# Kernel optimization log

Measured on AMD Instinct MI355X. Metric: run time of the kernel, lower is better.

Reference implementation:

```python
import jax, jax.numpy as jnp
from jax import lax
import numpy as np

NUM_BLOCK, NUM_LAYER = 4, 10
DILATIONS = [2 ** (i % NUM_LAYER) for i in range(NUM_BLOCK * NUM_LAYER)]


def setup_inputs() -> dict:
    key = jax.random.key(0)
    ks = jax.random.split(key, 6)
    s = 0.05
    return {
        "x": jax.random.normal(ks[0], (8, 256, 16000), dtype=jnp.float32),
        "W_start": jax.random.normal(ks[1], (32, 256), dtype=jnp.float32) * s,
        "W_dil": jax.random.normal(ks[2], (40, 128, 32, 2), dtype=jnp.float32) * s,
        "W_res": jax.random.normal(ks[3], (40, 32, 128), dtype=jnp.float32) * s,
        "W_e1": jax.random.normal(ks[4], (256, 32), dtype=jnp.float32) * s,
        "W_e2": jax.random.normal(ks[5], (256, 256), dtype=jnp.float32) * s,
    }


def _causal_dilated_conv(x, w, dilation):
    # x: [B, Cin, T], w: [Cout, Cin, K=2]. Left-pad (K-1)*dilation -> causal,
    # equivalent to torch symmetric-pad-then-trim-right.
    pad = (w.shape[-1] - 1) * dilation
    return lax.conv_general_dilated(
        x, w, window_strides=(1,), padding=[(pad, 0)],
        rhs_dilation=(dilation,), dimension_numbers=("NCH", "OIH", "NCH"))


def reference(x, W_start, W_dil, W_res, W_e1, W_e2):
    # start 1x1 conv (no bias)
    residual = jnp.einsum("oc,bct->bot", W_start, x)  # [B,32,T]
    skips = jnp.zeros_like(residual)
    for i, d in enumerate(DILATIONS):
        h = _causal_dilated_conv(residual, W_dil[i], d)       # [B,128,T]
        g = jnp.tanh(h) * jax.nn.sigmoid(h)                   # gated activation
        skip = jnp.einsum("oc,bct->bot", W_res[i], g)         # 1x1 -> [B,32,T]
        residual = residual + skip
        skips = skips + skip
    h = jax.nn.relu(skips)
    h = jax.nn.relu(jnp.einsum("oc,bct->bot", W_e1, h))       # [B,256,T]
    logits = jnp.einsum("oc,bct->bot", W_e2, h)               # [B,256,T]
    return logits
```

## Files before the change

kernel.cpp:

```cpp
#include <hip/hip_runtime.h>
#include <math.h>

#define T_LEN 16000
#define NTILE 250
#define TT 64
#define NBLK 2000
#define LGRID 500

static const int N_RES = 8 * 32 * T_LEN;

typedef _Float16 half_t;
typedef __attribute__((ext_vector_type(8))) _Float16 halfx8;
typedef __attribute__((ext_vector_type(4))) _Float16 halfx4;
typedef __attribute__((ext_vector_type(16))) float f32x16;
typedef unsigned int uint32;
typedef unsigned short ushort16;

#define MFMA(a, b, c) __builtin_amdgcn_mfma_f32_32x32x16_f16((a), (b), (c), 0, 0, 0)

static __device__ inline uint32 packpair(float a, float b) {
  half_t ha = (half_t)a, hb = (half_t)b;
  return (uint32)__builtin_bit_cast(ushort16, ha) |
         ((uint32)__builtin_bit_cast(ushort16, hb) << 16);
}

__global__ __launch_bounds__(256) void repack_k(
    const float* __restrict__ Wd, const float* __restrict__ Wr,
    const float* __restrict__ Ws, const float* __restrict__ We1,
    const float* __restrict__ We2,
    half_t* __restrict__ WaG, half_t* __restrict__ WrG, float* __restrict__ WsT,
    half_t* __restrict__ We1S, half_t* __restrict__ We2S) {
  int i = blockIdx.x * 256 + threadIdx.x;
  if (i < 40 * 128 * 128) {
    int l = i >> 14, r = i & 16383, o = r >> 7, k = r & 127;
    int kk = k & 63, c = kk >> 1, s = kk & 1;
    float w = Wd[(((l * 128 + o) * 32 + c) << 1) + s];
    half_t w0 = (half_t)w;
    WaG[i] = (k < 64) ? w0 : (half_t)((w - (float)w0) * 2048.f);
  }
  if (i < 40 * 32 * 256) {
    int l = i >> 13, r = i & 8191, o2 = r >> 8, k = r & 255;
    int kk = k & 127;
    int ks = kk >> 4, lh = (kk >> 3) & 1, j = kk & 7;
    int mh = ks >> 2, til = (ks >> 1) & 1, ab = ks & 1;
    int m = mh * 64 + til * 32 + ab * 16 + (j & 3) + ((j >> 2) << 3) + lh * 4;
    float w = Wr[(l * 32 + o2) * 128 + m];
    half_t w0 = (half_t)w;
    WrG[i] = (k < 128) ? w0 : (half_t)((w - (float)w0) * 2048.f);
  }
  if (i < 8192) {
    int c = i >> 5, o = i & 31;
    WsT[i] = Ws[o * 256 + c];
  }
  if (i < 16384) {
    int o = i >> 6, k = i & 63;
    float w = We1[o * 32 + (k & 31)];
    half_t w0 = (half_t)w;
    We1S[i] = (k < 32) ? w0 : (half_t)((w - (float)w0) * 2048.f);
  }
  if (i < 131072) {
    int o = i >> 9, k = i & 511;
    float w = We2[o * 256 + (k & 255)];
    half_t w0 = (half_t)w;
    We2S[i] = (k < 256) ? w0 : (half_t)((w - (float)w0) * 2048.f);
  }
}

__global__ __launch_bounds__(256) void start_k(const float* __restrict__ x,
                                               const float* __restrict__ WsT,
                                               float* __restrict__ res) {
  __shared__ float xs[32][68];
  int b = blockIdx.x / NTILE;
  int t0 = (blockIdx.x % NTILE) * TT;
  int tid = threadIdx.x;
  int o = tid & 31, tg = (tid >> 5) * 8;
  int lr = tid >> 3, lt = (tid & 7) * 8;
  float acc[8];
#pragma unroll
  for (int j = 0; j < 8; ++j) acc[j] = 0.f;
  for (int cc = 0; cc < 8; ++cc) {
    __syncthreads();
    const float* xp = x + ((size_t)b * 256 + cc * 32 + lr) * T_LEN + t0 + lt;
    *(float4*)&xs[lr][lt]     = *(const float4*)xp;
    *(float4*)&xs[lr][lt + 4] = *(const float4*)(xp + 4);
    __syncthreads();
#pragma unroll 4
    for (int c = 0; c < 32; ++c) {
      float w = WsT[(cc * 32 + c) * 32 + o];
      const float* xr = &xs[c][tg];
#pragma unroll
      for (int j = 0; j < 8; ++j) acc[j] += w * xr[j];
    }
  }
  float* rp = res + ((size_t)b * 32 + o) * T_LEN + t0 + tg;
  *(float4*)rp       = make_float4(acc[0], acc[1], acc[2], acc[3]);
  *(float4*)(rp + 4) = make_float4(acc[4], acc[5], acc[6], acc[7]);
}

__global__ __launch_bounds__(256, 3) void layer_k(const float* __restrict__ resIn,
                                                  float* __restrict__ resOut,
                                                  const half_t* __restrict__ WaL,
                                                  const half_t* __restrict__ WrL, int d) {
  __shared__ __align__(16) char sm[26112];
  const int ZT_OFF = 0, SKB_OFF = 0, CUR_OFF = 17408;
  int tid = threadIdx.x;
  int wave = tid >> 6, lane = tid & 63;
  int l31 = lane & 31, lhi = lane >> 5;
  int mh = wave & 1, nh = wave >> 1;

  for (int ti = 0; ti < 4; ++ti) {
    int tile = blockIdx.x + ti * LGRID;
    int b = tile / NTILE;
    int t0 = (tile - b * NTILE) * TT;

    {
      int c = tid >> 3, tw = (tid & 7) * 8;
      const float* rip = resIn + ((size_t)b * 32 + c) * T_LEN;
      float cv[8], pv[8];
      *(float4*)cv       = *(const float4*)(rip + t0 + tw);
      *(float4*)(cv + 4) = *(const float4*)(rip + t0 + tw + 4);
      int tp = t0 + tw - d;
      if (tp >= 0 && (d & 3) == 0) {
        *(float4*)pv       = *(const float4*)(rip + tp);
        *(float4*)(pv + 4) = *(const float4*)(rip + tp + 4);
      } else {
#pragma unroll
        for (int j = 0; j < 8; ++j) {
          int q = tp + j;
          pv[j] = (q >= 0) ? rip[q] : 0.f;
        }
      }
      float* cw = (float*)(sm + CUR_OFF) + c * 68 + tw;
      *(float4*)cw       = *(const float4*)cv;
      *(float4*)(cw + 4) = *(const float4*)(cv + 4);
#pragma unroll
      for (int j = 0; j < 8; ++j) {
        int t = tw + j;
        int sw = ((t >> 3) & 3) << 5;
        char* zrow = sm + ZT_OFF + t * 272;
        half_t p0 = (half_t)pv[j];
        half_t c0 = (half_t)cv[j];
        float pl = (pv[j] - (float)p0) * 2048.f;
        float cl = (cv[j] - (float)c0) * 2048.f;
        *(uint32*)(zrow + ((c * 4) ^ sw))       = packpair(pv[j], cv[j]);
        *(uint32*)(zrow + ((c * 4 + 128) ^ sw)) = packpair(pl, cl);
      }
    }
    __syncthreads();

    halfx8 a1h0[4], a1l0[4], a1h1[4], a1l1[4];
    {
      const half_t* wa = WaL + (mh * 64 + l31) * 128 + lhi * 8;
#pragma unroll
      for (int j = 0; j < 4; ++j) {
        a1h0[j] = *(const halfx8*)(wa + j * 16);
        a1l0[j] = *(const halfx8*)(wa + 64 + j * 16);
        a1h1[j] = *(const halfx8*)(wa + 32 * 128 + j * 16);
        a1l1[j] = *(const halfx8*)(wa + 32 * 128 + 64 + j * 16);
      }
    }

    f32x16 hi0{}, hi1{}, lo0{}, lo1{};
    {
      int colt = nh * 32 + l31;
      int sw = ((colt >> 3) & 3) << 5;
      const char* zr = sm + ZT_OFF + colt * 272;
#pragma unroll
      for (int ks = 0; ks < 12; ++ks) {
        int brow = (ks < 4) ? ks * 16 : ((ks < 8) ? (ks & 3) * 16 + 64 : (ks & 3) * 16);
        halfx8 bf = *(const halfx8*)(zr + ((brow * 2 + lhi * 16) ^ sw));
        if (ks < 4) {
          hi0 = MFMA(a1h0[ks], bf, hi0);
          hi1 = MFMA(a1h1[ks], bf, hi1);
        } else if (ks < 8) {
          lo0 = MFMA(a1h0[ks & 3], bf, lo0);
          lo1 = MFMA(a1h1[ks & 3], bf, lo1);
        } else {
          lo0 = MFMA(a1l0[ks & 3], bf, lo0);
          lo1 = MFMA(a1l1[ks & 3], bf, lo1);
        }
      }
    }

    halfx8 wrHi[4], wrLo[4];
    {
      const half_t* wr = WrL + l31 * 256 + mh * 64 + lhi * 8;
#pragma unroll
      for (int q = 0; q < 4; ++q) {
        wrHi[q] = *(const halfx8*)(wr + q * 16);
        wrLo[q] = *(const halfx8*)(wr + 128 + q * 16);
      }
    }

    halfx8 gh0a, gh0b, gl0a, gl0b, gh1a, gh1b, gl1a, gl1b;
    {
#pragma unroll
      for (int r = 0; r < 16; ++r) {
        float ha = hi0[r] + lo0[r] * (1.f / 2048.f);
        float hb = hi1[r] + lo1[r] * (1.f / 2048.f);
        ha = fmaxf(ha, -30.f);
        hb = fmaxf(hb, -30.f);
        float ea = __expf(-ha), eb = __expf(-hb);
        float ga = (1.f - ea) * __builtin_amdgcn_rcpf(1.f + ea * ea);
        float gb = (1.f - eb) * __builtin_amdgcn_rcpf(1.f + eb * eb);
        half_t ga0 = (half_t)ga;
        half_t gb0 = (half_t)gb;
        half_t ga1 = (half_t)((ga - (float)ga0) * 2048.f);
        half_t gb1 = (half_t)((gb - (float)gb0) * 2048.f);
        if (r < 8) {
          gh0a[r] = ga0; gl0a[r] = ga1; gh1a[r] = gb0; gl1a[r] = gb1;
        } else {
          gh0b[r - 8] = ga0; gl0b[r - 8] = ga1; gh1b[r - 8] = gb0; gl1b[r - 8] = gb1;
        }
      }
    }

    f32x16 shi{}, slo{};
    {
      shi = MFMA(wrHi[0], gh0a, shi);
      shi = MFMA(wrHi[1], gh0b, shi);
      shi = MFMA(wrHi[2], gh1a, shi);
      shi = MFMA(wrHi[3], gh1b, shi);
      slo = MFMA(wrHi[0], gl0a, slo);
      slo = MFMA(wrHi[1], gl0b, slo);
      slo = MFMA(wrHi[2], gl1a, slo);
      slo = MFMA(wrHi[3], gl1b, slo);
      slo = MFMA(wrLo[0], gh0a, slo);
      slo = MFMA(wrLo[1], gh0b, slo);
      slo = MFMA(wrLo[2], gh1a, slo);
      slo = MFMA(wrLo[3], gh1b, slo);
    }
    __syncthreads();

    {
      float* skb = (float*)(sm + SKB_OFF) + mh * 32 * 68;
#pragma unroll
      for (int r = 0; r < 16; ++r) {
        int row = (r & 3) + 8 * (r >> 2) + 4 * lhi;
        skb[row * 68 + nh * 32 + l31] = shi[r] + slo[r] * (1.f / 2048.f);
      }
    }
    __syncthreads();

    {
      int c = tid >> 3, tw = (tid & 7) * 8;
      const float* s0 = (const float*)(sm + SKB_OFF) + c * 68 + tw;
      const float* s1 = s0 + 32 * 68;
      const float* cu = (const float*)(sm + CUR_OFF) + c * 68 + tw;
      size_t base = ((size_t)b * 32 + c) * T_LEN + t0 + tw;
#pragma unroll
      for (int v = 0; v < 8; v += 4) {
        float4 sa = *(const float4*)(s0 + v);
        float4 sb = *(const float4*)(s1 + v);
        float4 cv = *(const float4*)(cu + v);
        float4 o;
        o.x = cv.x + sa.x + sb.x;
        o.y = cv.y + sa.y + sb.y;
        o.z = cv.z + sa.z + sb.z;
        o.w = cv.w + sa.w + sb.w;
        *(float4*)(resOut + base + v) = o;
      }
    }
    __syncthreads();
  }
}

__global__ __launch_bounds__(512) void end_k(const float* __restrict__ resF,
                                             const float* __restrict__ res0,
                                             const half_t* __restrict__ We1S,
                                             const half_t* __restrict__ We2S,
                                             float* __restrict__ out) {
  __shared__ __align__(16) char sm[75776];
  const int H2T_OFF = 0, H1F_OFF = 0, H1T_OFF = 66560;
  int tid = threadIdx.x;
  int b = blockIdx.x / NTILE;
  int t0 = (blockIdx.x % NTILE) * TT;

  {
    int c = tid >> 4, tt4 = (tid & 15) * 4;
    size_t base = ((size_t)b * 32 + c) * T_LEN + t0 + tt4;
    float4 f = *(const float4*)(resF + base);
    float4 z = *(const float4*)(res0 + base);
    float* h1 = (float*)(sm + H1F_OFF) + c * 68 + tt4;
    h1[0] = fmaxf(f.x - z.x, 0.f);
    h1[1] = fmaxf(f.y - z.y, 0.f);
    h1[2] = fmaxf(f.z - z.z, 0.f);
    h1[3] = fmaxf(f.w - z.w, 0.f);
  }
  __syncthreads();
  {
    int t = tid & 63, cg = tid >> 6;
    const float* h1 = (const float*)(sm + H1F_OFF);
    halfx4 hi, lo;
#pragma unroll
    for (int j = 0; j < 4; ++j) {
      float v = h1[(cg * 4 + j) * 68 + t];
      half_t h = (half_t)v;
      hi[j] = h;
      lo[j] = (half_t)((v - (float)h) * 2048.f);
    }
    half_t* h1t = (half_t*)(sm + H1T_OFF) + t * 72;
    *(halfx4*)(h1t + cg * 4)      = hi;
    *(halfx4*)(h1t + 32 + cg * 4) = lo;
  }
  __syncthreads();

  int wave = tid >> 6, lane = tid & 63;
  int l31 = lane & 31, lhi = lane >> 5;

  f32x16 aHi0{}, aHi1{}, aLo0{}, aLo1{};
  {
    const char* h1t = sm + H1T_OFF;
    const half_t* wp = We1S + (wave * 32 + l31) * 64;
#pragma unroll
    for (int ks = 0; ks < 2; ++ks) {
      halfx8 hiA = *(const halfx8*)(wp + ks * 16 + lhi * 8);
      halfx8 loA = *(const halfx8*)(wp + 32 + ks * 16 + lhi * 8);
      const char* br0 = h1t + l31 * 144;
      const char* br1 = h1t + (32 + l31) * 144;
      halfx8 hiB0 = *(const halfx8*)(br0 + (ks * 16 + lhi * 8) * 2);
      halfx8 loB0 = *(const halfx8*)(br0 + (32 + ks * 16 + lhi * 8) * 2);
      halfx8 hiB1 = *(const halfx8*)(br1 + (ks * 16 + lhi * 8) * 2);
      halfx8 loB1 = *(const halfx8*)(br1 + (32 + ks * 16 + lhi * 8) * 2);
      aHi0 = MFMA(hiA, hiB0, aHi0);
      aLo0 = MFMA(hiA, loB0, aLo0);
      aLo0 = MFMA(loA, hiB0, aLo0);
      aHi1 = MFMA(hiA, hiB1, aHi1);
      aLo1 = MFMA(hiA, loB1, aLo1);
      aLo1 = MFMA(loA, hiB1, aLo1);
    }
  }
  {
#pragma unroll
    for (int n = 0; n < 2; ++n) {
      const f32x16& aH = n ? aHi1 : aHi0;
      const f32x16& aL = n ? aLo1 : aLo0;
      int t = n * 32 + l31;
      half_t* row = (half_t*)(sm + H2T_OFF) + t * 520;
#pragma unroll
      for (int g = 0; g < 4; ++g) {
        halfx4 hi, lo;
#pragma unroll
        for (int j = 0; j < 4; ++j) {
          int r = g * 4 + j;
          float v = aH[r] + aL[r] * (1.f / 2048.f);
          v = fmaxf(v, 0.f);
          half_t h = (half_t)v;
          hi[j] = h;
          lo[j] = (half_t)((v - (float)h) * 2048.f);
        }
        int col = wave * 32 + g * 8 + lhi * 4;
        *(halfx4*)(row + col)       = hi;
        *(halfx4*)(row + 256 + col) = lo;
      }
    }
  }
  __syncthreads();

  f32x16 bHi0{}, bHi1{}, bLo0{}, bLo1{};
  {
    const half_t* wp = We2S + (size_t)(wave * 32 + l31) * 512;
    const char* h2t = sm + H2T_OFF;
#pragma unroll 2
    for (int ks = 0; ks < 16; ++ks) {
      halfx8 hiA = *(const halfx8*)(wp + ks * 16 + lhi * 8);
      halfx8 loA = *(const halfx8*)(wp + 256 + ks * 16 + lhi * 8);
      const char* br0 = h2t + l31 * 1040;
      const char* br1 = h2t + (32 + l31) * 1040;
      halfx8 hiB0 = *(const halfx8*)(br0 + (ks * 16 + lhi * 8) * 2);
      halfx8 loB0 = *(const halfx8*)(br0 + (256 + ks * 16 + lhi * 8) * 2);
      halfx8 hiB1 = *(const halfx8*)(br1 + (ks * 16 + lhi * 8) * 2);
      halfx8 loB1 = *(const halfx8*)(br1 + (256 + ks * 16 + lhi * 8) * 2);
      bHi0 = MFMA(hiA, hiB0, bHi0);
      bLo0 = MFMA(hiA, loB0, bLo0);
      bLo0 = MFMA(loA, hiB0, bLo0);
      bHi1 = MFMA(hiA, hiB1, bHi1);
      bLo1 = MFMA(hiA, loB1, bLo1);
      bLo1 = MFMA(loA, hiB1, bLo1);
    }
  }
  {
#pragma unroll
    for (int n = 0; n < 2; ++n) {
      const f32x16& bH = n ? bHi1 : bHi0;
      const f32x16& bL = n ? bLo1 : bLo0;
      int t = t0 + n * 32 + l31;
#pragma unroll
      for (int r = 0; r < 16; ++r) {
        int o = wave * 32 + (r & 3) + 8 * (r >> 2) + 4 * lhi;
        out[((size_t)b * 256 + o) * T_LEN + t] = bH[r] + bL[r] * (1.f / 2048.f);
      }
    }
  }
}

extern "C" void kernel_launch(void* const* d_in, const int* in_sizes, int n_in,
                              void* d_out, int out_size, void* d_ws, size_t ws_size,
                              hipStream_t stream) {
  const float* x   = (const float*)d_in[0];
  const float* Wst = (const float*)d_in[1];
  const float* Wd  = (const float*)d_in[2];
  const float* Wr  = (const float*)d_in[3];
  const float* We1 = (const float*)d_in[4];
  const float* We2 = (const float*)d_in[5];
  float* out = (float*)d_out;
  float* ws = (float*)d_ws;

  float* resA = ws;
  float* resB = resA + N_RES;
  float* resC = resB + N_RES;
  half_t* WaG  = (half_t*)(resC + N_RES);
  half_t* WrG  = WaG + 40 * 16384;
  float*  WsT  = (float*)(WrG + 40 * 8192);
  half_t* We1S = (half_t*)(WsT + 8192);
  half_t* We2S = We1S + 16384;

  repack_k<<<2560, 256, 0, stream>>>(Wd, Wr, Wst, We1, We2, WaG, WrG, WsT, We1S, We2S);
  start_k<<<NBLK, 256, 0, stream>>>(x, WsT, resA);

  const float* rin = resA;
  for (int l = 0; l < 40; ++l) {
    float* rout = (l & 1) ? resC : resB;
    layer_k<<<LGRID, 256, 0, stream>>>(rin, rout, WaG + l * 16384, WrG + l * 8192,
                                       1 << (l % 10));
    rin = rout;
  }
  end_k<<<NBLK, 512, 0, stream>>>(rin, resA, We1S, We2S, out);
}
```

Before: 1.183 ms.

## Prefetch next tile's residual into registers and hoist weight loads out of tile loop

The per-layer kernel now loads the layer weights into registers once, before the tile loop, instead of reloading them for every tile. It double-buffers the current and previous-time residual values in registers, so the global load for the next tile is issued while the MFMA work on the current tile runs. The residual is kept in registers rather than a shared-memory copy, which shrinks LDS use. Launch bounds drop from 3 to 2 blocks per SM to leave room for the extra registers, which may reduce occupancy.

```diff
diff --git a/kernel.cpp b/kernel.cpp
--- a/kernel.cpp
+++ b/kernel.cpp
@@ -97,172 +97,177 @@
   *(float4*)(rp + 4) = make_float4(acc[4], acc[5], acc[6], acc[7]);
 }
 
-__global__ __launch_bounds__(256, 3) void layer_k(const float* __restrict__ resIn,
+#define LOAD_TILE(TI, CV, PV)                                              \
+  {                                                                        \
+    int tl_ = blockIdx.x + (TI) * LGRID;                                   \
+    int bb_ = tl_ / NTILE;                                                 \
+    int tb_ = (tl_ - bb_ * NTILE) * TT;                                    \
+    const float* rip_ = resIn + ((size_t)bb_ * 32 + cth) * T_LEN;          \
+    *(float4*)(CV)       = *(const float4*)(rip_ + tb_ + twh);             \
+    *(float4*)((CV) + 4) = *(const float4*)(rip_ + tb_ + twh + 4);         \
+    int tp_ = tb_ + twh - d;                                               \
+    if (tp_ >= 0 && (d & 3) == 0) {                                        \
+      *(float4*)(PV)       = *(const float4*)(rip_ + tp_);                 \
+      *(float4*)((PV) + 4) = *(const float4*)(rip_ + tp_ + 4);             \
+    } else {                                                               \
+      _Pragma("unroll")                                                    \
+      for (int j_ = 0; j_ < 8; ++j_) {                                     \
+        int q_ = tp_ + j_;                                                 \
+        (PV)[j_] = (q_ >= 0) ? rip_[q_] : 0.f;                             \
+      }                                                                    \
+    }                                                                      \
+  }
+
+#define TILE_BODY(TI, CV, PV, NCV, NPV, PREF)                                  \
+  {                                                                            \
+    int tile = blockIdx.x + (TI) * LGRID;                                      \
+    int b = tile / NTILE;                                                      \
+    int t0 = (tile - b * NTILE) * TT;                                          \
+                                             \
+    _Pragma("unroll")                                                          \
+    for (int j = 0; j < 8; ++j) {                                              \
+      int t = twh + j;                                                         \
+      int sw = ((t >> 3) & 3) << 5;                                            \
+      char* zrow = sm + t * 272;                                               \
+      half_t p0 = (half_t)(PV)[j];                                             \
+      half_t c0 = (half_t)(CV)[j];                                             \
+      float pl = ((PV)[j] - (float)p0) * 2048.f;                               \
+      float cl = ((CV)[j] - (float)c0) * 2048.f;                               \
+      *(uint32*)(zrow + ((cth * 4) ^ sw))       = packpair((PV)[j], (CV)[j]);  \
+      *(uint32*)(zrow + ((cth * 4 + 128) ^ sw)) = packpair(pl, cl);            \
+    }                                                                          \
+    __syncthreads();                                                           \
+       \
+    if (PREF) { LOAD_TILE((TI) + 1, NCV, NPV); }                               \
+                                      \
+    f32x16 hi0{}, hi1{}, lo0{}, lo1{};                                         \
+    {                                                                          \
+      int colt = nh * 32 + l31;                                                \
+      int sw = ((colt >> 3) & 3) << 5;                                         \
+      const char* zr = sm + colt * 272;                                        \
+      _Pragma("unroll")                                                        \
+      for (int ks = 0; ks < 12; ++ks) {                                        \
+        int brow = (ks < 4) ? ks * 16                                          \
+                            : ((ks < 8) ? (ks & 3) * 16 + 64 : (ks & 3) * 16); \
+        halfx8 bf = *(const halfx8*)(zr + ((brow * 2 + lhi * 16) ^ sw));       \
+        if (ks < 4) {                                                          \
+          hi0 = MFMA(a1h0[ks], bf, hi0);                                       \
+          hi1 = MFMA(a1h1[ks], bf, hi1);                                       \
+        } else if (ks < 8) {                                                   \
+          lo0 = MFMA(a1h0[ks & 3], bf, lo0);                                   \
+          lo1 = MFMA(a1h1[ks & 3], bf, lo1);                                   \
+        } else {                                                               \
+          lo0 = MFMA(a1l0[ks & 3], bf, lo0);                                   \
+          lo1 = MFMA(a1l1[ks & 3], bf, lo1);                                   \
+        }                                                                      \
+      }                                                                        \
+    }                                                                          \
+                          \
+    halfx8 gh0a, gh0b, gl0a, gl0b, gh1a, gh1b, gl1a, gl1b;                     \
+    _Pragma("unroll")                                                          \
+    for (int r = 0; r < 16; ++r) {                                             \
+      float ha = hi0[r] + lo0[r] * (1.f / 2048.f);                             \
+      float hb = hi1[r] + lo1[r] * (1.f / 2048.f);                             \
+      ha = fmaxf(ha, -30.f);                                                   \
+      hb = fmaxf(hb, -30.f);                                                   \
+      float ea = __expf(-ha), eb = __expf(-hb);                                \
+      float ga = (1.f - ea) * __builtin_amdgcn_rcpf(1.f + ea * ea);            \
+      float gb = (1.f - eb) * __builtin_amdgcn_rcpf(1.f + eb * eb);            \
+      half_t ga0 = (half_t)ga;                                                 \
+      half_t gb0 = (half_t)gb;                                                 \
+      half_t ga1 = (half_t)((ga - (float)ga0) * 2048.f);                       \
+      half_t gb1 = (half_t)((gb - (float)gb0) * 2048.f);                       \
+      if (r < 8) {                                                             \
+        gh0a[r] = ga0; gl0a[r] = ga1; gh1a[r] = gb0; gl1a[r] = gb1;            \
+      } else {                                                                 \
+        gh0b[r - 8] = ga0; gl0b[r - 8] = ga1;                                  \
+        gh1b[r - 8] = gb0; gl1b[r - 8] = gb1;                                  \
+      }                                                                        \
+    }                                                                          \
+                         \
+    f32x16 shi{}, slo{};                                                       \
+    shi = MFMA(wrHi[0], gh0a, shi);                                            \
+    shi = MFMA(wrHi[1], gh0b, shi);                                            \
+    shi = MFMA(wrHi[2], gh1a, shi);                                            \
+    shi = MFMA(wrHi[3], gh1b, shi);                                            \
+    slo = MFMA(wrHi[0], gl0a, slo);                                            \
+    slo = MFMA(wrHi[1], gl0b, slo);                                            \
+    slo = MFMA(wrHi[2], gl1a, slo);                                            \
+    slo = MFMA(wrHi[3], gl1b, slo);                                            \
+    slo = MFMA(wrLo[0], gh0a, slo);                                            \
+    slo = MFMA(wrLo[1], gh0b, slo);                                            \
+    slo = MFMA(wrLo[2], gh1a, slo);                                            \
+    slo = MFMA(wrLo[3], gh1b, slo);                                            \
+    __syncthreads();                      \
+    {                                                                          \
+      float* skb = (float*)sm + mh * 32 * 68;                                  \
+      _Pragma("unroll")                                                        \
+      for (int r = 0; r < 16; ++r) {                                           \
+        int row = (r & 3) + 8 * (r >> 2) + 4 * lhi;                            \
+        skb[row * 68 + nh * 32 + l31] = shi[r] + slo[r] * (1.f / 2048.f);      \
+      }                                                                        \
+    }                                                                          \
+    __syncthreads();                                                           \
+                     \
+    {                                                                          \
+      const float* s0 = (const float*)sm + cth * 68 + twh;                     \
+      const float* s1 = s0 + 32 * 68;                                          \
+      size_t base = ((size_t)b * 32 + cth) * T_LEN + t0 + twh;                 \
+      _Pragma("unroll")                                                        \
+      for (int v = 0; v < 8; v += 4) {                                         \
+        float4 sa = *(const float4*)(s0 + v);                                  \
+        float4 sb = *(const float4*)(s1 + v);                                  \
+        float4 o;                                                              \
+        o.x = (CV)[v]     + sa.x + sb.x;                                       \
+        o.y = (CV)[v + 1] + sa.y + sb.y;                                       \
+        o.z = (CV)[v + 2] + sa.z + sb.z;                                       \
+        o.w = (CV)[v + 3] + sa.w + sb.w;                                       \
+        *(float4*)(resOut + base + v) = o;                                     \
+      }                                                                        \
+    }                                                                          \
+    __syncthreads();       \
+  }
+
+__global__ __launch_bounds__(256, 2) void layer_k(const float* __restrict__ resIn,
                                                   float* __restrict__ resOut,
                                                   const half_t* __restrict__ WaL,
-                                                  const half_t* __restrict__ WrL, int d) {
-  __shared__ __align__(16) char sm[26112];
-  const int ZT_OFF = 0, SKB_OFF = 0, CUR_OFF = 17408;
+                                                  const half_t* __restrict__ WrL,
+                                                  int d) {
+  __shared__ __align__(16) char sm[17408];
   int tid = threadIdx.x;
   int wave = tid >> 6, lane = tid & 63;
   int l31 = lane & 31, lhi = lane >> 5;
   int mh = wave & 1, nh = wave >> 1;
-
-  for (int ti = 0; ti < 4; ++ti) {
-    int tile = blockIdx.x + ti * LGRID;
-    int b = tile / NTILE;
-    int t0 = (tile - b * NTILE) * TT;
-
-    {
-      int c = tid >> 3, tw = (tid & 7) * 8;
-      const float* rip = resIn + ((size_t)b * 32 + c) * T_LEN;
-      float cv[8], pv[8];
-      *(float4*)cv       = *(const float4*)(rip + t0 + tw);
-      *(float4*)(cv + 4) = *(const float4*)(rip + t0 + tw + 4);
-      int tp = t0 + tw - d;
-      if (tp >= 0 && (d & 3) == 0) {
-        *(float4*)pv       = *(const float4*)(rip + tp);
-        *(float4*)(pv + 4) = *(const float4*)(rip + tp + 4);
-      } else {
-#pragma unroll
-        for (int j = 0; j < 8; ++j) {
-          int q = tp + j;
-          pv[j] = (q >= 0) ? rip[q] : 0.f;
-        }
-      }
-      float* cw = (float*)(sm + CUR_OFF) + c * 68 + tw;
-      *(float4*)cw       = *(const float4*)cv;
-      *(float4*)(cw + 4) = *(const float4*)(cv + 4);
-#pragma unroll
-      for (int j = 0; j < 8; ++j) {
-        int t = tw + j;
-        int sw = ((t >> 3) & 3) << 5;
-        char* zrow = sm + ZT_OFF + t * 272;
-        half_t p0 = (half_t)pv[j];
-        half_t c0 = (half_t)cv[j];
-        float pl = (pv[j] - (float)p0) * 2048.f;
-        float cl = (cv[j] - (float)c0) * 2048.f;
-        *(uint32*)(zrow + ((c * 4) ^ sw))       = packpair(pv[j], cv[j]);
-        *(uint32*)(zrow + ((c * 4 + 128) ^ sw)) = packpair(pl, cl);
-      }
-    }
-    __syncthreads();
-
-    halfx8 a1h0[4], a1l0[4], a1h1[4], a1l1[4];
-    {
-      const half_t* wa = WaL + (mh * 64 + l31) * 128 + lhi * 8;
-#pragma unroll
-      for (int j = 0; j < 4; ++j) {
-        a1h0[j] = *(const halfx8*)(wa + j * 16);
-        a1l0[j] = *(const halfx8*)(wa + 64 + j * 16);
-        a1h1[j] = *(const halfx8*)(wa + 32 * 128 + j * 16);
-        a1l1[j] = *(const halfx8*)(wa + 32 * 128 + 64 + j * 16);
-      }
-    }
-
-    f32x16 hi0{}, hi1{}, lo0{}, lo1{};
-    {
-      int colt = nh * 32 + l31;
-      int sw = ((colt >> 3) & 3) << 5;
-      const char* zr = sm + ZT_OFF + colt * 272;
-#pragma unroll
-      for (int ks = 0; ks < 12; ++ks) {
-        int brow = (ks < 4) ? ks * 16 : ((ks < 8) ? (ks & 3) * 16 + 64 : (ks & 3) * 16);
-        halfx8 bf = *(const halfx8*)(zr + ((brow * 2 + lhi * 16) ^ sw));
-        if (ks < 4) {
-          hi0 = MFMA(a1h0[ks], bf, hi0);
-          hi1 = MFMA(a1h1[ks], bf, hi1);
-        } else if (ks < 8) {
-          lo0 = MFMA(a1h0[ks & 3], bf, lo0);
-          lo1 = MFMA(a1h1[ks & 3], bf, lo1);
-        } else {
-          lo0 = MFMA(a1l0[ks & 3], bf, lo0);
-          lo1 = MFMA(a1l1[ks & 3], bf, lo1);
-        }
-      }
-    }
-
-    halfx8 wrHi[4], wrLo[4];
-    {
-      const half_t* wr = WrL + l31 * 256 + mh * 64 + lhi * 8;
-#pragma unroll
-      for (int q = 0; q < 4; ++q) {
-        wrHi[q] = *(const halfx8*)(wr + q * 16);
-        wrLo[q] = *(const halfx8*)(wr + 128 + q * 16);
-      }
-    }
-
-    halfx8 gh0a, gh0b, gl0a, gl0b, gh1a, gh1b, gl1a, gl1b;
-    {
-#pragma unroll
-      for (int r = 0; r < 16; ++r) {
-        float ha = hi0[r] + lo0[r] * (1.f / 2048.f);
-        float hb = hi1[r] + lo1[r] * (1.f / 2048.f);
-        ha = fmaxf(ha, -30.f);
-        hb = fmaxf(hb, -30.f);
-        float ea = __expf(-ha), eb = __expf(-hb);
-        float ga = (1.f - ea) * __builtin_amdgcn_rcpf(1.f + ea * ea);
-        float gb = (1.f - eb) * __builtin_amdgcn_rcpf(1.f + eb * eb);
-        half_t ga0 = (half_t)ga;
-        half_t gb0 = (half_t)gb;
-        half_t ga1 = (half_t)((ga - (float)ga0) * 2048.f);
-        half_t gb1 = (half_t)((gb - (float)gb0) * 2048.f);
-        if (r < 8) {
-          gh0a[r] = ga0; gl0a[r] = ga1; gh1a[r] = gb0; gl1a[r] = gb1;
-        } else {
-          gh0b[r - 8] = ga0; gl0b[r - 8] = ga1; gh1b[r - 8] = gb0; gl1b[r - 8] = gb1;
-        }
-      }
-    }
-
-    f32x16 shi{}, slo{};
-    {
-      shi = MFMA(wrHi[0], gh0a, shi);
-      shi = MFMA(wrHi[1], gh0b, shi);
-      shi = MFMA(wrHi[2], gh1a, shi);
-      shi = MFMA(wrHi[3], gh1b, shi);
-      slo = MFMA(wrHi[0], gl0a, slo);
-      slo = MFMA(wrHi[1], gl0b, slo);
-      slo = MFMA(wrHi[2], gl1a, slo);
-      slo = MFMA(wrHi[3], gl1b, slo);
-      slo = MFMA(wrLo[0], gh0a, slo);
-      slo = MFMA(wrLo[1], gh0b, slo);
-      slo = MFMA(wrLo[2], gh1a, slo);
-      slo = MFMA(wrLo[3], gh1b, slo);
-    }
-    __syncthreads();
-
-    {
-      float* skb = (float*)(sm + SKB_OFF) + mh * 32 * 68;
-#pragma unroll
-      for (int r = 0; r < 16; ++r) {
-        int row = (r & 3) + 8 * (r >> 2) + 4 * lhi;
-        skb[row * 68 + nh * 32 + l31] = shi[r] + slo[r] * (1.f / 2048.f);
-      }
-    }
-    __syncthreads();
-
-    {
-      int c = tid >> 3, tw = (tid & 7) * 8;
-      const float* s0 = (const float*)(sm + SKB_OFF) + c * 68 + tw;
-      const float* s1 = s0 + 32 * 68;
-      const float* cu = (const float*)(sm + CUR_OFF) + c * 68 + tw;
-      size_t base = ((size_t)b * 32 + c) * T_LEN + t0 + tw;
-#pragma unroll
-      for (int v = 0; v < 8; v += 4) {
-        float4 sa = *(const float4*)(s0 + v);
-        float4 sb = *(const float4*)(s1 + v);
-        float4 cv = *(const float4*)(cu + v);
-        float4 o;
-        o.x = cv.x + sa.x + sb.x;
-        o.y = cv.y + sa.y + sb.y;
-        o.z = cv.z + sa.z + sb.z;
-        o.w = cv.w + sa.w + sb.w;
-        *(float4*)(resOut + base + v) = o;
-      }
-    }
-    __syncthreads();
-  }
+  int cth = tid >> 3, twh = (tid & 7) * 8;
+
+  halfx8 a1h0[4], a1l0[4], a1h1[4], a1l1[4];
+  {
+    const half_t* wa = WaL + (mh * 64 + l31) * 128 + lhi * 8;
+#pragma unroll
+    for (int j = 0; j < 4; ++j) {
+      a1h0[j] = *(const halfx8*)(wa + j * 16);
+      a1l0[j] = *(const halfx8*)(wa + 64 + j * 16);
+      a1h1[j] = *(const halfx8*)(wa + 32 * 128 + j * 16);
+      a1l1[j] = *(const halfx8*)(wa + 32 * 128 + 64 + j * 16);
+    }
+  }
+  halfx8 wrHi[4], wrLo[4];
+  {
+    const half_t* wr = WrL + l31 * 256 + mh * 64 + lhi * 8;
+#pragma unroll
+    for (int q = 0; q < 4; ++q) {
+      wrHi[q] = *(const halfx8*)(wr + q * 16);
+      wrLo[q] = *(const halfx8*)(wr + 128 + q * 16);
+    }
+  }
+
+  float cvA[8], pvA[8], cvB[8], pvB[8];
+  LOAD_TILE(0, cvA, pvA);
+
+  TILE_BODY(0, cvA, pvA, cvB, pvB, 1)
+  TILE_BODY(1, cvB, pvB, cvA, pvA, 1)
+  TILE_BODY(2, cvA, pvA, cvB, pvB, 1)
+  TILE_BODY(3, cvB, pvB, cvA, pvA, 0)
 }
 
 __global__ __launch_bounds__(512) void end_k(const float* __restrict__ resF,
@@ -289,19 +294,19 @@
   }
   __syncthreads();
   {
-    int t = tid & 63, cg = tid >> 6;
+    int t = tid & 63, cg2 = tid >> 6;
     const float* h1 = (const float*)(sm + H1F_OFF);
     halfx4 hi, lo;
 #pragma unroll
     for (int j = 0; j < 4; ++j) {
-      float v = h1[(cg * 4 + j) * 68 + t];
+      float v = h1[(cg2 * 4 + j) * 68 + t];
       half_t h = (half_t)v;
       hi[j] = h;
       lo[j] = (half_t)((v - (float)h) * 2048.f);
     }
     half_t* h1t = (half_t*)(sm + H1T_OFF) + t * 72;
-    *(halfx4*)(h1t + cg * 4)      = hi;
-    *(halfx4*)(h1t + 32 + cg * 4) = lo;
+    *(halfx4*)(h1t + cg2 * 4)      = hi;
+    *(halfx4*)(h1t + 32 + cg2 * 4) = lo;
   }
   __syncthreads();
 
```

Result: faster. 1.050 ms (-11.2%).
